# Performance work log

Measured on AMD Instinct MI355X. Metric: run time of the kernel, lower is better.

The kernel has to match this reference:

```python
import jax, jax.numpy as jnp
import numpy as np

BETA = 0.25
B, N, D = 8, 4096, 256
NUM_CODES = 4096


def setup_inputs() -> dict:
    key = jax.random.key(0)
    kx, kc = jax.random.split(key)
    x = jax.random.normal(kx, (B, N, D), dtype=jnp.float32)
    # matches nn.init.uniform_(weight, -1/dim, 1/dim)
    codebook = jax.random.uniform(kc, (NUM_CODES, D), dtype=jnp.float32,
                                  minval=-1.0 / D, maxval=1.0 / D)
    return {"x": x, "codebook": codebook}


def reference(x, codebook):
    b, n, d = x.shape
    flat = x.reshape(b * n, d)                                   # [BN, D]
    # squared euclidean distances: ||z||^2 - 2 z.e^T + ||e||^2   # [BN, K]
    distances = (jnp.sum(flat * flat, axis=1, keepdims=True)
                 - 2.0 * jnp.einsum('md,kd->mk', flat, codebook)
                 + jnp.sum(codebook * codebook, axis=1)[None, :])
    indices = jnp.argmin(distances, axis=1)                      # [BN]
    z_q = codebook[indices].reshape(b, n, d)                     # [B, N, D]
    # commitment + codebook losses (detach == stop_gradient)
    sg = jax.lax.stop_gradient
    loss = jnp.mean((sg(z_q) - x) ** 2) + BETA * jnp.mean((z_q - sg(x)) ** 2)
    # straight-through estimator
    z_q_st = x + sg(z_q - x)
    return z_q_st, loss, indices.reshape(b, n)
```

## Files before the change

### kernel.cpp

```cpp
#include <hip/hip_runtime.h>

#define MTOT 32768
#define KC   4096
#define DDIM 256
#define BM   128
#define ZELEMS (MTOT * DDIM)
#define THRESH 2.0e-4f
#define WLCAP 8192
#define RGRID 2048

typedef _Float16 half8 __attribute__((ext_vector_type(8)));
typedef float f32x4 __attribute__((ext_vector_type(4)));

__device__ __forceinline__ void gload_lds16(const void* g, void* l) {
  __builtin_amdgcn_global_load_lds(
      (const __attribute__((address_space(1))) void*)g,
      (__attribute__((address_space(3))) void*)l, 16, 0, 0);
}

__device__ __forceinline__ float sqr_rn(float v) { return __fmul_rn(v, v); }

__global__ __launch_bounds__(256) void vq_prep2(const float* __restrict__ x,
                                                const float* __restrict__ cb,
                                                float* __restrict__ S,
                                                float* __restrict__ cnorm,
                                                _Float16* __restrict__ cbsw,
                                                int* __restrict__ wl_count,
                                                double* __restrict__ accum) {
  const int t = threadIdx.x;
  if (blockIdx.x == 0 && t == 0) { *accum = 0.0; *wl_count = 0; }
  const int sub = t >> 4, lane16 = t & 15;
  const int h = lane16 >> 3, j = lane16 & 7;
  const bool isrow = blockIdx.x < 2048;
  const int idx = (isrow ? blockIdx.x : blockIdx.x - 2048) * 16 + sub;
  const float* p = (isrow ? x + (size_t)idx * DDIM : cb + (size_t)idx * DDIM);

  float r = 0.f;
  const float* q = p + h * 128 + j;
#pragma unroll
  for (int i = 0; i < 16; ++i) r = __fadd_rn(r, sqr_rn(q[i * 8]));
  r = __fadd_rn(r, __shfl_xor(r, 1, 64));
  r = __fadd_rn(r, __shfl_xor(r, 2, 64));
  r = __fadd_rn(r, __shfl_xor(r, 4, 64));
  float sv = __fadd_rn(r, __shfl_xor(r, 8, 64));
  if (lane16 == 0) {
    if (isrow) S[idx] = sv; else cnorm[idx] = sv;
  }

  if (!isrow) {
    const int sw = idx & 7;
    _Float16* dst = cbsw + (size_t)idx * DDIM;
#pragma unroll
    for (int c = 0; c < 2; ++c) {
      int jj = lane16 + c * 16;
      float4 a4 = *reinterpret_cast<const float4*>(p + jj * 8);
      float4 b4 = *reinterpret_cast<const float4*>(p + jj * 8 + 4);
      union { half8 v; _Float16 hh[8]; } u;
      u.hh[0] = (_Float16)(a4.x * 256.0f); u.hh[1] = (_Float16)(a4.y * 256.0f);
      u.hh[2] = (_Float16)(a4.z * 256.0f); u.hh[3] = (_Float16)(a4.w * 256.0f);
      u.hh[4] = (_Float16)(b4.x * 256.0f); u.hh[5] = (_Float16)(b4.y * 256.0f);
      u.hh[6] = (_Float16)(b4.z * 256.0f); u.hh[7] = (_Float16)(b4.w * 256.0f);
      *reinterpret_cast<half8*>(dst + ((jj ^ sw) * 8)) = u.v;
    }
  }
}

__global__ __launch_bounds__(512, 2) void vq_score(const float* __restrict__ x,
                                                   const float* __restrict__ cbf,
                                                   const _Float16* __restrict__ cbsw,
                                                   const float* __restrict__ Sarr,
                                                   const float* __restrict__ cnorm,
                                                   int* __restrict__ wl,
                                                   int* __restrict__ wl_count,
                                                   double* __restrict__ accum,
                                                   float* __restrict__ out) {
  __shared__ _Float16 cbt[2][64 * DDIM];
  __shared__ float cn[KC];
  __shared__ float scrV1[4][BM];
  __shared__ float scrV2[4][BM];
  __shared__ int   scrI1[4][BM];
  __shared__ int   idx_sh[BM];
  __shared__ float wred[8];

  const int t = threadIdx.x;
  const int m0 = blockIdx.x * BM;
  const int lane = t & 63, w = t >> 6;
  const int rg = w >> 2, cg = w & 3;
  const int lo = lane & 15, hi = lane >> 4;

#pragma unroll
  for (int j = 0; j < 4; ++j)
    gload_lds16(cbsw + 0 * 16384 + w * 2048 + j * 512 + lane * 8,
                &cbt[0][w * 2048 + j * 512]);
#pragma unroll
  for (int j = 0; j < 4; ++j)
    gload_lds16(cbsw + 1 * 16384 + w * 2048 + j * 512 + lane * 8,
                &cbt[1][w * 2048 + j * 512]);

#pragma unroll
  for (int i = 0; i < 2; ++i) {
    int fi = t + i * 512;
    *reinterpret_cast<float4*>(&cn[fi * 4]) =
        *reinterpret_cast<const float4*>(cnorm + fi * 4);
  }

  half8 a[4][8];
#pragma unroll
  for (int s2 = 0; s2 < 4; ++s2) {
    const float* xr = x + (size_t)(m0 + rg * 64 + s2 * 16 + lo) * DDIM + hi * 8;
#pragma unroll
    for (int s = 0; s < 8; ++s) {
      float4 u0 = *reinterpret_cast<const float4*>(xr + s * 32);
      float4 u1 = *reinterpret_cast<const float4*>(xr + s * 32 + 4);
      union { half8 v; _Float16 h[8]; } uu;
      uu.h[0] = (_Float16)u0.x; uu.h[1] = (_Float16)u0.y;
      uu.h[2] = (_Float16)u0.z; uu.h[3] = (_Float16)u0.w;
      uu.h[4] = (_Float16)u1.x; uu.h[5] = (_Float16)u1.y;
      uu.h[6] = (_Float16)u1.z; uu.h[7] = (_Float16)u1.w;
      a[s2][s] = uu.v;
    }
  }

  const int code_l = cg * 16 + lo;
  const int bswz = (lo & 7) << 3;

  float v1[4][4], v2[4][4]; int i1[4][4];
#pragma unroll
  for (int s2 = 0; s2 < 4; ++s2)
#pragma unroll
    for (int r = 0; r < 4; ++r) { v1[s2][r] = 3.4e38f; v2[s2][r] = 3.4e38f; i1[s2][r] = 0; }

  __syncthreads();

  for (int kt = 0; kt < KC / 64; ++kt) {
    const int cur = kt & 1;
    if (kt < KC / 64 - 1) asm volatile("s_waitcnt vmcnt(4)" ::: "memory");
    else                  asm volatile("s_waitcnt vmcnt(0)" ::: "memory");
    __builtin_amdgcn_s_barrier();

    const float C = cn[kt * 64 + code_l];
    f32x4 acc[4];
#pragma unroll
    for (int s2 = 0; s2 < 4; ++s2) acc[s2] = (f32x4){0.f, 0.f, 0.f, 0.f};
#pragma unroll
    for (int s = 0; s < 8; ++s) {
      half8 b = *reinterpret_cast<half8*>(
          &cbt[cur][(code_l * DDIM + s * 32 + hi * 8) ^ bswz]);
      acc[0] = __builtin_amdgcn_mfma_f32_16x16x32_f16(a[0][s], b, acc[0], 0, 0, 0);
      acc[1] = __builtin_amdgcn_mfma_f32_16x16x32_f16(a[1][s], b, acc[1], 0, 0, 0);
      acc[2] = __builtin_amdgcn_mfma_f32_16x16x32_f16(a[2][s], b, acc[2], 0, 0, 0);
      acc[3] = __builtin_amdgcn_mfma_f32_16x16x32_f16(a[3][s], b, acc[3], 0, 0, 0);
    }
    const int code = kt * 64 + code_l;
#pragma unroll
    for (int s2 = 0; s2 < 4; ++s2) {
#pragma unroll
      for (int r = 0; r < 4; ++r) {
        float sv = fmaf(acc[s2][r], -0.0078125f, C);
        float mx = fmaxf(v1[s2][r], sv);
        v2[s2][r] = fminf(v2[s2][r], mx);
        bool lt = sv < v1[s2][r];
        if (lt) { v1[s2][r] = sv; i1[s2][r] = code; }
      }
    }

    __builtin_amdgcn_s_barrier();
    if (kt < KC / 64 - 2) {
#pragma unroll
      for (int j = 0; j < 4; ++j)
        gload_lds16(cbsw + (size_t)(kt + 2) * 16384 + w * 2048 + j * 512 + lane * 8,
                    &cbt[cur][w * 2048 + j * 512]);
    }
  }

#pragma unroll
  for (int s2 = 0; s2 < 4; ++s2) {
#pragma unroll
    for (int r = 0; r < 4; ++r) {
      float v = v1[s2][r], u = v2[s2][r]; int ii = i1[s2][r];
#pragma unroll
      for (int m = 1; m <= 8; m <<= 1) {
        float ov = __shfl_xor(v, m, 64);
        int   oi = __shfl_xor(ii, m, 64);
        float ou = __shfl_xor(u, m, 64);
        float mx = fmaxf(v, ov);
        u = fminf(fminf(u, ou), mx);
        bool take = (ov < v) || (ov == v && oi < ii);
        if (take) { v = ov; ii = oi; }
      }
      if (lo == 0) {
        int rowl = rg * 64 + s2 * 16 + hi * 4 + r;
        scrV1[cg][rowl] = v;
        scrV2[cg][rowl] = u;
        scrI1[cg][rowl] = ii;
      }
    }
  }
  __syncthreads();

  float part = 0.f;
  if (t < BM) {
    float bv1 = 3.4e38f, bv2 = 3.4e38f; int bi1 = 0x7fffffff;
#pragma unroll
    for (int c = 0; c < 4; ++c) {
      float v = scrV1[c][t];
      float u = scrV2[c][t];
      int  ii = scrI1[c][t];
      float mx = fmaxf(bv1, v);
      bv2 = fminf(fminf(bv2, u), mx);
      if (v < bv1 || (v == bv1 && ii < bi1)) { bv1 = v; bi1 = ii; }
    }
    int row = m0 + t;
    idx_sh[t] = bi1;
    out[(size_t)ZELEMS + 1 + row] = (float)bi1;
    float gap = bv2 - bv1;
    if (gap <= THRESH) {
      int pos = atomicAdd(wl_count, 1);
      if (pos >= WLCAP) part = __fadd_rn(Sarr[row], bv1);
      else wl[pos] = row;
    } else {
      part = __fadd_rn(Sarr[row], bv1);
    }
  }
#pragma unroll
  for (int off = 32; off >= 1; off >>= 1) part += __shfl_down(part, off, 64);
  if (lane == 0) wred[w] = part;
  __syncthreads();
  if (t == 0) {
    double s = 0.0;
#pragma unroll
    for (int i = 0; i < 8; ++i) s += (double)wred[i];
    atomicAdd(accum, s);
  }

#pragma unroll
  for (int i = 0; i < 16; ++i) {
    int fi = t + i * 512;
    int row = fi >> 6, dc = fi & 63;
    int code = idx_sh[row];
    float4 c4 = *reinterpret_cast<const float4*>(cbf + (size_t)code * DDIM + dc * 4);
    float4 x4 = *reinterpret_cast<const float4*>(x + (size_t)(m0 + row) * DDIM + dc * 4);
    float4 o;
    o.x = __fadd_rn(x4.x, __fsub_rn(c4.x, x4.x));
    o.y = __fadd_rn(x4.y, __fsub_rn(c4.y, x4.y));
    o.z = __fadd_rn(x4.z, __fsub_rn(c4.z, x4.z));
    o.w = __fadd_rn(x4.w, __fsub_rn(c4.w, x4.w));
    *reinterpret_cast<float4*>(out + (size_t)(m0 + row) * DDIM + dc * 4) = o;
  }
}

__global__ __launch_bounds__(256) void vq_rescore(const float* __restrict__ x,
                                                  const float* __restrict__ cb,
                                                  const float* __restrict__ Sarr,
                                                  const float* __restrict__ cnorm,
                                                  const int* __restrict__ wl,
                                                  const int* __restrict__ wl_count,
                                                  float* __restrict__ pD,
                                                  int* __restrict__ pI) {
  const int cnt = min(*wl_count, WLCAP);
  if (cnt == 0) return;
  const int ngroups = (cnt + 7) >> 3;
  const int nitems = ngroups * 16;

  __shared__ float xs[8][260];
  __shared__ int rsh[8];
  __shared__ float scrv[8][4];
  __shared__ int   scri[8][4];

  const int t = threadIdx.x;
  const int lane = t & 63, w = t >> 6;

  for (int item = blockIdx.x; item < nitems; item += RGRID) {
    const int g = item >> 4, chunk = item & 15;
    __syncthreads();
    if (t < 8) { int e = g * 8 + t; rsh[t] = wl[(e < cnt) ? e : g * 8]; }
    __syncthreads();
#pragma unroll
    for (int j = 0; j < 2; ++j) {
      int fi = t + j * 256, i = fi >> 6, dq = fi & 63;
      *reinterpret_cast<float4*>(&xs[i][dq * 4]) =
          *reinterpret_cast<const float4*>(x + (size_t)rsh[i] * DDIM + dq * 4);
    }
    __syncthreads();

    const int code = chunk * 256 + t;
    const float* cp = cb + (size_t)code * DDIM;
    const float C = cnorm[code];

    float acc[8][4];
#pragma unroll
    for (int i = 0; i < 8; ++i)
#pragma unroll
      for (int l = 0; l < 4; ++l) acc[i][l] = 0.f;

#pragma unroll 4
    for (int dq = 0; dq < 64; ++dq) {
      float4 cv = *reinterpret_cast<const float4*>(cp + dq * 4);
#pragma unroll
      for (int i = 0; i < 8; ++i) {
        float4 xv = *reinterpret_cast<float4*>(&xs[i][dq * 4]);
        acc[i][0] = __fadd_rn(acc[i][0], __fmul_rn(xv.x, cv.x));
        acc[i][1] = __fadd_rn(acc[i][1], __fmul_rn(xv.y, cv.y));
        acc[i][2] = __fadd_rn(acc[i][2], __fmul_rn(xv.z, cv.z));
        acc[i][3] = __fadd_rn(acc[i][3], __fmul_rn(xv.w, cv.w));
      }
    }

#pragma unroll
    for (int i = 0; i < 8; ++i) {
      float e = __fadd_rn(__fadd_rn(acc[i][0], acc[i][1]),
                          __fadd_rn(acc[i][2], acc[i][3]));
      float Sv = Sarr[rsh[i]];
      float D = __fadd_rn(__fsub_rn(Sv, __fmul_rn(2.0f, e)), C);
      float v = D; int ii = code;
#pragma unroll
      for (int m = 1; m <= 32; m <<= 1) {
        float ov = __shfl_xor(v, m, 64);
        int   oi = __shfl_xor(ii, m, 64);
        if (ov < v || (ov == v && oi < ii)) { v = ov; ii = oi; }
      }
      if (lane == 0) { scrv[i][w] = v; scri[i][w] = ii; }
    }
    __syncthreads();
    if (t < 8) {
      float bv = 3.4e38f; int bi = 0x7fffffff;
#pragma unroll
      for (int c = 0; c < 4; ++c) {
        float v = scrv[t][c]; int ii = scri[t][c];
        if (v < bv || (v == bv && ii < bi)) { bv = v; bi = ii; }
      }
      int rpos = g * 8 + t;
      if (rpos < cnt) { pD[rpos * 16 + chunk] = bv; pI[rpos * 16 + chunk] = bi; }
    }
  }
}

__global__ __launch_bounds__(256) void vq_combine2(const float* __restrict__ x,
                                                   const float* __restrict__ cb,
                                                   const int* __restrict__ wl,
                                                   const int* __restrict__ wl_count,
                                                   const float* __restrict__ pD,
                                                   const int* __restrict__ pI,
                                                   float* __restrict__ out,
                                                   double* __restrict__ accum) {
  __shared__ int fixi[WLCAP];
  __shared__ double dred[4];
  const int cnt = min(*wl_count, WLCAP);
  const int t = threadIdx.x;

  double s = 0.0;
  for (int r = t; r < cnt; r += 256) {
    float bv = 3.4e38f; int bi = 0x7fffffff;
#pragma unroll
    for (int c = 0; c < 16; ++c) {
      float v = pD[r * 16 + c]; int ii = pI[r * 16 + c];
      if (v < bv || (v == bv && ii < bi)) { bv = v; bi = ii; }
    }
    fixi[r] = bi;
    out[(size_t)ZELEMS + 1 + wl[r]] = (float)bi;
    s += (double)bv;
  }
#pragma unroll
  for (int off = 32; off >= 1; off >>= 1) s += __shfl_down(s, off, 64);
  if ((t & 63) == 0) dred[t >> 6] = s;
  __syncthreads();
  if (t == 0) {
    double tot = (dred[0] + dred[1]) + (dred[2] + dred[3]);
    double prev = atomicAdd(accum, tot);
    out[ZELEMS] = (float)(1.25 * (prev + tot) / (double)ZELEMS);
  }

  for (int f = t; f < cnt * 64; f += 256) {
    int r = f >> 6, dc = f & 63;
    int row = wl[r], code = fixi[r];
    float4 c4 = *reinterpret_cast<const float4*>(cb + (size_t)code * DDIM + dc * 4);
    float4 x4 = *reinterpret_cast<const float4*>(x + (size_t)row * DDIM + dc * 4);
    float4 o;
    o.x = __fadd_rn(x4.x, __fsub_rn(c4.x, x4.x));
    o.y = __fadd_rn(x4.y, __fsub_rn(c4.y, x4.y));
    o.z = __fadd_rn(x4.z, __fsub_rn(c4.z, x4.z));
    o.w = __fadd_rn(x4.w, __fsub_rn(c4.w, x4.w));
    *reinterpret_cast<float4*>(out + (size_t)row * DDIM + dc * 4) = o;
  }
}

extern "C" void kernel_launch(void* const* d_in, const int* in_sizes, int n_in,
                              void* d_out, int out_size, void* d_ws, size_t ws_size,
                              hipStream_t stream) {
  const float* x  = (const float*)d_in[0];
  const float* cb = (const float*)d_in[1];
  float* out = (float*)d_out;

  char* ws = (char*)d_ws;
  float*     S        = (float*)(ws + 0);
  float*     cnorm    = (float*)(ws + 131072);
  int*       wl       = (int*)  (ws + 278528);
  int*       wl_count = (int*)  (ws + 311296);
  double*    accum    = (double*)(ws + 311312);
  float*     pD       = (float*)(ws + 315392);
  int*       pI       = (int*)  (ws + 839680);
  _Float16*  cbsw     = (_Float16*)(ws + 1363968);

  vq_prep2<<<2304, 256, 0, stream>>>(x, cb, S, cnorm, cbsw, wl_count, accum);
  vq_score<<<MTOT / BM, 512, 0, stream>>>(x, cb, cbsw, S, cnorm, wl, wl_count, accum, out);
  vq_rescore<<<RGRID, 256, 0, stream>>>(x, cb, S, cnorm, wl, wl_count, pD, pI);
  vq_combine2<<<1, 256, 0, stream>>>(x, cb, wl, wl_count, pD, pI, out, accum);
}
```

Before: 189.6 us.

## Move z_q output emission out of score kernel into separate emit kernel

New measurement: 164.2 us. 13.4% less time.

```diff
diff --git a/kernel.cpp b/kernel.cpp
--- a/kernel.cpp
+++ b/kernel.cpp
@@ -66,20 +66,18 @@
 }
 
 __global__ __launch_bounds__(512, 2) void vq_score(const float* __restrict__ x,
-                                                   const float* __restrict__ cbf,
                                                    const _Float16* __restrict__ cbsw,
                                                    const float* __restrict__ Sarr,
                                                    const float* __restrict__ cnorm,
+                                                   int* __restrict__ bestidx,
                                                    int* __restrict__ wl,
                                                    int* __restrict__ wl_count,
-                                                   double* __restrict__ accum,
-                                                   float* __restrict__ out) {
+                                                   double* __restrict__ accum) {
   __shared__ _Float16 cbt[2][64 * DDIM];
   __shared__ float cn[KC];
   __shared__ float scrV1[4][BM];
   __shared__ float scrV2[4][BM];
   __shared__ int   scrI1[4][BM];
-  __shared__ int   idx_sh[BM];
   __shared__ float wred[8];
 
   const int t = threadIdx.x;
@@ -211,8 +209,7 @@
       if (v < bv1 || (v == bv1 && ii < bi1)) { bv1 = v; bi1 = ii; }
     }
     int row = m0 + t;
-    idx_sh[t] = bi1;
-    out[(size_t)ZELEMS + 1 + row] = (float)bi1;
+    bestidx[row] = bi1;
     float gap = bv2 - bv1;
     if (gap <= THRESH) {
       int pos = atomicAdd(wl_count, 1);
@@ -231,21 +228,6 @@
 #pragma unroll
     for (int i = 0; i < 8; ++i) s += (double)wred[i];
     atomicAdd(accum, s);
-  }
-
-#pragma unroll
-  for (int i = 0; i < 16; ++i) {
-    int fi = t + i * 512;
-    int row = fi >> 6, dc = fi & 63;
-    int code = idx_sh[row];
-    float4 c4 = *reinterpret_cast<const float4*>(cbf + (size_t)code * DDIM + dc * 4);
-    float4 x4 = *reinterpret_cast<const float4*>(x + (size_t)(m0 + row) * DDIM + dc * 4);
-    float4 o;
-    o.x = __fadd_rn(x4.x, __fsub_rn(c4.x, x4.x));
-    o.y = __fadd_rn(x4.y, __fsub_rn(c4.y, x4.y));
-    o.z = __fadd_rn(x4.z, __fsub_rn(c4.z, x4.z));
-    o.w = __fadd_rn(x4.w, __fsub_rn(c4.w, x4.w));
-    *reinterpret_cast<float4*>(out + (size_t)(m0 + row) * DDIM + dc * 4) = o;
   }
 }
 
@@ -335,15 +317,13 @@
   }
 }
 
-__global__ __launch_bounds__(256) void vq_combine2(const float* __restrict__ x,
-                                                   const float* __restrict__ cb,
-                                                   const int* __restrict__ wl,
-                                                   const int* __restrict__ wl_count,
-                                                   const float* __restrict__ pD,
-                                                   const int* __restrict__ pI,
-                                                   float* __restrict__ out,
-                                                   double* __restrict__ accum) {
-  __shared__ int fixi[WLCAP];
+__global__ __launch_bounds__(256) void vq_combine(const int* __restrict__ wl,
+                                                  const int* __restrict__ wl_count,
+                                                  const float* __restrict__ pD,
+                                                  const int* __restrict__ pI,
+                                                  int* __restrict__ bestidx,
+                                                  double* __restrict__ accum,
+                                                  float* __restrict__ out) {
   __shared__ double dred[4];
   const int cnt = min(*wl_count, WLCAP);
   const int t = threadIdx.x;
@@ -356,8 +336,7 @@
       float v = pD[r * 16 + c]; int ii = pI[r * 16 + c];
       if (v < bv || (v == bv && ii < bi)) { bv = v; bi = ii; }
     }
-    fixi[r] = bi;
-    out[(size_t)ZELEMS + 1 + wl[r]] = (float)bi;
+    bestidx[wl[r]] = bi;
     s += (double)bv;
   }
 #pragma unroll
@@ -369,18 +348,34 @@
     double prev = atomicAdd(accum, tot);
     out[ZELEMS] = (float)(1.25 * (prev + tot) / (double)ZELEMS);
   }
-
-  for (int f = t; f < cnt * 64; f += 256) {
-    int r = f >> 6, dc = f & 63;
-    int row = wl[r], code = fixi[r];
+}
+
+__global__ __launch_bounds__(256) void vq_emit(const float* __restrict__ x,
+                                               const float* __restrict__ cb,
+                                               const int* __restrict__ bestidx,
+                                               float* __restrict__ out) {
+  __shared__ int ish[64];
+  const int t = threadIdx.x;
+  const int m0 = blockIdx.x * 64;
+  if (t < 64) {
+    int ii = bestidx[m0 + t];
+    ish[t] = ii;
+    out[(size_t)ZELEMS + 1 + m0 + t] = (float)ii;
+  }
+  __syncthreads();
+#pragma unroll
+  for (int i = 0; i < 16; ++i) {
+    int fi = t + i * 256;
+    int row = fi >> 6, dc = fi & 63;
+    int code = ish[row];
     float4 c4 = *reinterpret_cast<const float4*>(cb + (size_t)code * DDIM + dc * 4);
-    float4 x4 = *reinterpret_cast<const float4*>(x + (size_t)row * DDIM + dc * 4);
+    float4 x4 = *reinterpret_cast<const float4*>(x + (size_t)(m0 + row) * DDIM + dc * 4);
     float4 o;
     o.x = __fadd_rn(x4.x, __fsub_rn(c4.x, x4.x));
     o.y = __fadd_rn(x4.y, __fsub_rn(c4.y, x4.y));
     o.z = __fadd_rn(x4.z, __fsub_rn(c4.z, x4.z));
     o.w = __fadd_rn(x4.w, __fsub_rn(c4.w, x4.w));
-    *reinterpret_cast<float4*>(out + (size_t)row * DDIM + dc * 4) = o;
+    *reinterpret_cast<float4*>(out + (size_t)(m0 + row) * DDIM + dc * 4) = o;
   }
 }
 
@@ -394,6 +389,7 @@
   char* ws = (char*)d_ws;
   float*     S        = (float*)(ws + 0);
   float*     cnorm    = (float*)(ws + 131072);
+  int*       bestidx  = (int*)  (ws + 147456);
   int*       wl       = (int*)  (ws + 278528);
   int*       wl_count = (int*)  (ws + 311296);
   double*    accum    = (double*)(ws + 311312);
@@ -402,7 +398,8 @@
   _Float16*  cbsw     = (_Float16*)(ws + 1363968);
 
   vq_prep2<<<2304, 256, 0, stream>>>(x, cb, S, cnorm, cbsw, wl_count, accum);
-  vq_score<<<MTOT / BM, 512, 0, stream>>>(x, cb, cbsw, S, cnorm, wl, wl_count, accum, out);
+  vq_score<<<MTOT / BM, 512, 0, stream>>>(x, cbsw, S, cnorm, bestidx, wl, wl_count, accum);
   vq_rescore<<<RGRID, 256, 0, stream>>>(x, cb, S, cnorm, wl, wl_count, pD, pI);
-  vq_combine2<<<1, 256, 0, stream>>>(x, cb, wl, wl_count, pD, pI, out, accum);
-}
+  vq_combine<<<1, 256, 0, stream>>>(wl, wl_count, pD, pI, bestidx, accum, out);
+  vq_emit<<<MTOT / 64, 256, 0, stream>>>(x, cb, bestidx, out);
+}
```
